# Optimization experiments

Hardware: AMD Instinct MI355X
Metric: run time of the kernel (lower is better)

The kernel has to match this reference:

```python
import jax, jax.numpy as jnp
import numpy as np

# (multiplicity, irrep dim 2l+1, is_scalar) for '128x0e + 64x1o + 32x2e'
IRREPS = [(128, 1, True), (64, 3, False), (32, 5, False)]
EPS = 1e-05
NUM_GRAPHS = 64


def setup_inputs() -> dict:
    key = jax.random.key(0)
    k1, k2 = jax.random.split(key)
    N, dim = 200000, 480
    x = jax.random.normal(k1, (N, dim), dtype=jnp.float32)
    batch_id = jnp.sort(jax.random.randint(k2, (N,), 0, NUM_GRAPHS)).astype(jnp.int64)
    weight = jnp.ones((224,), dtype=jnp.float32)   # per-irrep-channel scale
    bias = jnp.zeros((128,), dtype=jnp.float32)    # scalar channels only
    return {"input": x, "batch_id_tensor": batch_id, "weight": weight, "bias": bias}


def _segment_mean(vals, seg, num_segments):
    # vals: (N, mul) -> per-graph mean (G, mul)
    sums = jax.ops.segment_sum(vals, seg, num_segments=num_segments)
    counts = jax.ops.segment_sum(jnp.ones((vals.shape[0],), vals.dtype), seg,
                                 num_segments=num_segments)
    return sums / jnp.maximum(counts, 1.0)[:, None]


def reference(input, batch_id_tensor, weight, bias):
    N = input.shape[0]
    seg = batch_id_tensor.astype(jnp.int32)
    ix = iw = ib = 0
    outs = []
    for mul, d, is_scalar in IRREPS:
        f = input[:, ix:ix + mul * d].reshape(N, mul, d)
        ix += mul * d
        if is_scalar:
            # instance norm: per-graph mean of scalar channels, gathered back
            m = _segment_mean(f[:, :, 0], seg, NUM_GRAPHS)[seg]  # (N, mul)
            f = f - m[:, :, None]
        # 'component' normalization: mean of squares over irrep dim
        fn = jnp.mean(f * f, axis=2)                             # (N, mul)
        # reduce='mean' over (trivial) spatial axis, then per-graph mean
        fn = _segment_mean(fn, seg, NUM_GRAPHS)[seg]             # (N, mul)
        fn = (fn + EPS) ** -0.5 * weight[iw:iw + mul]
        iw += mul
        f = f * fn[:, :, None]
        if is_scalar:
            f = f + bias[ib:ib + mul][:, None]
            ib += mul
        outs.append(f.reshape(N, mul * d))
    return jnp.concatenate(outs, axis=1)
```

## Files before the change

kernel.cpp:

```cpp
#include <hip/hip_runtime.h>

#define NGRAPHS 64
#define DIM 480
#define NCH 224
#define EPS 1e-5f
#define TILE 128

typedef float f32x4 __attribute__((ext_vector_type(4)));

#define OFF_SSQ   0
#define OFF_SUM   14336
#define OFF_START 22528
#define OFF_TPRE  22593
#define ZN_FLOATS 22528

__device__ __forceinline__ int col2ch(int col) {
    if (col < 128) return col;
    if (col < 320) return 128 + (col - 128) / 3;
    return 192 + (col - 320) / 5;
}

__global__ __launch_bounds__(256) void init_kernel(const int* __restrict__ bid,
                                                   float* __restrict__ ws, int N) {
    int b = blockIdx.x;
    if (b < 88) {
        int i = b * 256 + threadIdx.x;
        if (i < ZN_FLOATS) ws[i] = 0.0f;
        return;
    }
    int* start = (int*)(ws + OFF_START);
    int* tpre  = (int*)(ws + OFF_TPRE);
    int g = threadIdx.x;
    if (g <= NGRAPHS) {
        int lo = 0, hi = N;
        while (lo < hi) { int mid = (lo + hi) >> 1; if (bid[mid] < g) lo = mid + 1; else hi = mid; }
        start[g] = lo;
    }
    __syncthreads();
    if (threadIdx.x == 0) {
        int acc = 0;
        for (int gg = 0; gg < NGRAPHS; ++gg) {
            tpre[gg] = acc;
            acc += (start[gg + 1] - start[gg] + TILE - 1) / TILE;
        }
        tpre[NGRAPHS] = acc;
    }
}

__device__ __forceinline__ void block_tile(const int* __restrict__ tpre, int b,
                                           int& g, int& tile) {
    int lo = 0, hi = NGRAPHS;
    while (hi - lo > 1) {
        int mid = (lo + hi) >> 1;
        if (tpre[mid] <= b) lo = mid; else hi = mid;
    }
    g = lo;
    tile = b - tpre[lo];
}

__device__ __forceinline__ void flush_quad(float* __restrict__ SQ, int col0,
                                           float v0, float v1, float v2, float v3) {
    float v[4] = {v0, v1, v2, v3};
    int ch0 = col2ch(col0), ch1 = col2ch(col0 + 1),
        ch2 = col2ch(col0 + 2), ch3 = col2ch(col0 + 3);
    float acc = v[0]; int cur = ch0;
    if (ch1 == cur) acc += v[1]; else { atomicAdd(&SQ[cur], acc); cur = ch1; acc = v[1]; }
    if (ch2 == cur) acc += v[2]; else { atomicAdd(&SQ[cur], acc); cur = ch2; acc = v[2]; }
    if (ch3 == cur) acc += v[3]; else { atomicAdd(&SQ[cur], acc); cur = ch3; acc = v[3]; }
    atomicAdd(&SQ[cur], acc);
}

__global__ __launch_bounds__(256) void stats_kernel(const float* __restrict__ x,
                                                    float* __restrict__ ws) {
    __shared__ float red[256][13];
    const int* start = (const int*)(ws + OFF_START);
    const int* tpre  = (const int*)(ws + OFF_TPRE);
    if ((int)blockIdx.x >= tpre[NGRAPHS]) return;
    int g, tile;
    block_tile(tpre, blockIdx.x, g, tile);
    int r0 = start[g] + tile * TILE;
    int r1 = min(r0 + TILE, start[g + 1]);

    const int t  = threadIdx.x;
    const int tx = t & 63;
    const int ty = t >> 6;

    float ssq[8]  = {0, 0, 0, 0, 0, 0, 0, 0};
    float ssum[4] = {0, 0, 0, 0};
    for (int r = r0 + ty; r < r1; r += 4) {
        const float4* rowp = (const float4*)(x + (size_t)r * DIM);
        float4 v0 = rowp[tx];
        ssq[0] += v0.x * v0.x; ssq[1] += v0.y * v0.y;
        ssq[2] += v0.z * v0.z; ssq[3] += v0.w * v0.w;
        if (tx < 32) {
            ssum[0] += v0.x; ssum[1] += v0.y; ssum[2] += v0.z; ssum[3] += v0.w;
        }
        if (tx < 56) {
            float4 v1 = rowp[64 + tx];
            ssq[4] += v1.x * v1.x; ssq[5] += v1.y * v1.y;
            ssq[6] += v1.z * v1.z; ssq[7] += v1.w * v1.w;
        }
    }

#pragma unroll
    for (int j = 0; j < 8; ++j) red[t][j] = ssq[j];
#pragma unroll
    for (int j = 0; j < 4; ++j) red[t][8 + j] = ssum[j];
    __syncthreads();
    if (ty == 0) {
        float s[8], sm[4];
#pragma unroll
        for (int j = 0; j < 8; ++j)
            s[j] = red[tx][j] + red[tx + 64][j] + red[tx + 128][j] + red[tx + 192][j];
#pragma unroll
        for (int j = 0; j < 4; ++j)
            sm[j] = red[tx][8 + j] + red[tx + 64][8 + j] + red[tx + 128][8 + j] + red[tx + 192][8 + j];
        float* SQ = ws + OFF_SSQ + (size_t)g * NCH;
        float* SM = ws + OFF_SUM + (size_t)g * 128;
        flush_quad(SQ, 4 * tx, s[0], s[1], s[2], s[3]);
        if (tx < 32) {
#pragma unroll
            for (int j = 0; j < 4; ++j) atomicAdd(&SM[4 * tx + j], sm[j]);
        }
        if (tx < 56) flush_quad(SQ, 256 + 4 * tx, s[4], s[5], s[6], s[7]);
    }
}

__global__ __launch_bounds__(256) void norm_kernel(const float* __restrict__ x,
                                                   const float* __restrict__ w,
                                                   const float* __restrict__ bias,
                                                   const float* __restrict__ ws,
                                                   float* __restrict__ out) {
    const int* start = (const int*)(ws + OFF_START);
    const int* tpre  = (const int*)(ws + OFF_TPRE);
    int total = tpre[NGRAPHS];
    int b = total - 1 - (int)blockIdx.x;
    if (b < 0) return;
    int t = threadIdx.x;
    if (t >= 240) return;
    int g, tile;
    block_tile(tpre, b, g, tile);
    int r0 = start[g] + tile * TILE;
    int r1 = min(r0 + TILE, start[g + 1]);

    int row_off = t / 120;
    int c4 = t - row_off * 120;

    float cnt = (float)max(start[g + 1] - start[g], 1);
    const float* SQ = ws + OFF_SSQ + (size_t)g * NCH;
    const float* SM = ws + OFF_SUM + (size_t)g * 128;

    float A[4], B[4];
#pragma unroll
    for (int j = 0; j < 4; ++j) {
        int col = 4 * c4 + j;
        int ch = col2ch(col);
        float ssq = SQ[ch];
        if (col < 128) {
            float m   = SM[col] / cnt;
            float var = ssq / cnt - m * m;
            float Av  = rsqrtf(var + EPS) * w[ch];
            A[j] = Av;
            B[j] = bias[col] - m * Av;
        } else {
            float d = (col < 320) ? 3.0f : 5.0f;
            A[j] = rsqrtf(ssq / (d * cnt) + EPS) * w[ch];
            B[j] = 0.0f;
        }
    }

    const float4* xp = (const float4*)(x + (size_t)(r0 + row_off) * DIM) + c4;
    f32x4*        op = (f32x4*)(out + (size_t)(r0 + row_off) * DIM + 4 * c4);
    const int stride4 = 2 * (DIM / 4);
    for (int r = r0 + row_off; r < r1; r += 2) {
        float4 xv = *xp;
        f32x4 o;
        o.x = xv.x * A[0] + B[0];
        o.y = xv.y * A[1] + B[1];
        o.z = xv.z * A[2] + B[2];
        o.w = xv.w * A[3] + B[3];
        *op = o;
        xp += stride4;
        op += stride4;
    }
}

extern "C" void kernel_launch(void* const* d_in, const int* in_sizes, int n_in,
                              void* d_out, int out_size, void* d_ws, size_t ws_size,
                              hipStream_t stream) {
    const float* x   = (const float*)d_in[0];
    const int*   bid = (const int*)d_in[1];
    const float* w   = (const float*)d_in[2];
    const float* b   = (const float*)d_in[3];
    float* ws  = (float*)d_ws;
    float* out = (float*)d_out;
    int N = in_sizes[1];
    int ntiles_ub = (N + TILE - 1) / TILE + NGRAPHS;

    init_kernel<<<89, 256, 0, stream>>>(bid, ws, N);
    stats_kernel<<<ntiles_ub, 256, 0, stream>>>(x, ws);
    norm_kernel<<<ntiles_ub, 256, 0, stream>>>(x, w, b, ws, out);
}
```

Before: 273.2 us.

## Fuse stats and normalization into one persistent kernel with per-graph spin barrier

Replaces the init, stats and norm launches with a single kernel that launches 16 blocks per graph. Each block computes partial sums for its slice of rows and writes them to a per-block slot, then waits on a per-graph counter until all 16 slots are in. After that the block reduces the partials and normalizes the same rows it just read, which it expects to still find in cache. Output stores become nontemporal. The design needs all 1024 blocks to be co-resident for the spin barrier to be safe, has a bounded spin fallback, and loses load balance across graphs of uneven size.

```diff
diff --git a/kernel.cpp b/kernel.cpp
--- a/kernel.cpp
+++ b/kernel.cpp
@@ -4,21 +4,157 @@
 #define DIM 480
 #define NCH 224
 #define EPS 1e-5f
+#define SLOTS 16
+#define PSTR 640
+#define SPIN_BOUND (1u << 24)
 #define TILE 128
 
 typedef float f32x4 __attribute__((ext_vector_type(4)));
+
+__device__ __forceinline__ int col2ch(int col) {
+    if (col < 128) return col;
+    if (col < 320) return 128 + (col - 128) / 3;
+    return 192 + (col - 320) / 5;
+}
+
+__global__ __launch_bounds__(256, 4) void fused_kernel(
+        const float* __restrict__ x, const int* __restrict__ bid,
+        const float* __restrict__ w, const float* __restrict__ bias,
+        unsigned int* __restrict__ done, float* __restrict__ part,
+        float* __restrict__ out, int N) {
+    __shared__ int s_se[2];
+    __shared__ float red[256][13];
+    __shared__ float lds_col[608];
+
+    const int t  = threadIdx.x;
+    const int g  = blockIdx.x >> 4;
+    const int js = blockIdx.x & (SLOTS - 1);
+
+    if (t < 2) {
+        int target = g + t, lo = 0, hi = N;
+        while (lo < hi) { int mid = (lo + hi) >> 1; if (bid[mid] < target) lo = mid + 1; else hi = mid; }
+        s_se[t] = lo;
+    }
+    __syncthreads();
+    const int rs = s_se[0], re = s_se[1];
+    const int cnt_i = re - rs;
+    const int chunk = (cnt_i + SLOTS - 1) / SLOTS;
+    const int r0s = rs + js * chunk;
+    const int r1s = min(r0s + chunk, re);
+
+    const int tx = t & 63;
+    const int ty = t >> 6;
+
+    float ssq[8]  = {0, 0, 0, 0, 0, 0, 0, 0};
+    float ssum[4] = {0, 0, 0, 0};
+    for (int r = r0s + ty; r < r1s; r += 4) {
+        const float4* rowp = (const float4*)(x + (size_t)r * DIM);
+        float4 v0 = rowp[tx];
+        ssq[0] += v0.x * v0.x; ssq[1] += v0.y * v0.y;
+        ssq[2] += v0.z * v0.z; ssq[3] += v0.w * v0.w;
+        if (tx < 32) { ssum[0] += v0.x; ssum[1] += v0.y; ssum[2] += v0.z; ssum[3] += v0.w; }
+        if (tx < 56) {
+            float4 v1 = rowp[64 + tx];
+            ssq[4] += v1.x * v1.x; ssq[5] += v1.y * v1.y;
+            ssq[6] += v1.z * v1.z; ssq[7] += v1.w * v1.w;
+        }
+    }
+#pragma unroll
+    for (int j = 0; j < 8; ++j) red[t][j] = ssq[j];
+#pragma unroll
+    for (int j = 0; j < 4; ++j) red[t][8 + j] = ssum[j];
+    __syncthreads();
+    if (ty == 0) {
+        float* P = part + (size_t)blockIdx.x * PSTR;
+#pragma unroll
+        for (int j = 0; j < 8; ++j) ssq[j] = red[tx][j] + red[tx + 64][j] + red[tx + 128][j] + red[tx + 192][j];
+#pragma unroll
+        for (int j = 0; j < 4; ++j) ssum[j] = red[tx][8 + j] + red[tx + 64][8 + j] + red[tx + 128][8 + j] + red[tx + 192][8 + j];
+#pragma unroll
+        for (int j = 0; j < 4; ++j)
+            __hip_atomic_store(&P[4 * tx + j], ssq[j], __ATOMIC_RELAXED, __HIP_MEMORY_SCOPE_AGENT);
+        if (tx < 56) {
+#pragma unroll
+            for (int j = 0; j < 4; ++j)
+                __hip_atomic_store(&P[256 + 4 * tx + j], ssq[4 + j], __ATOMIC_RELAXED, __HIP_MEMORY_SCOPE_AGENT);
+        }
+        if (tx < 32) {
+#pragma unroll
+            for (int j = 0; j < 4; ++j)
+                __hip_atomic_store(&P[480 + 4 * tx + j], ssum[j], __ATOMIC_RELAXED, __HIP_MEMORY_SCOPE_AGENT);
+        }
+    }
+    __syncthreads();
+
+    if (t == 0) {
+        __hip_atomic_fetch_add(&done[g], 1u, __ATOMIC_RELEASE, __HIP_MEMORY_SCOPE_AGENT);
+        unsigned it = 0;
+        while (__hip_atomic_load(&done[g], __ATOMIC_ACQUIRE, __HIP_MEMORY_SCOPE_AGENT) < SLOTS) {
+            if (++it > SPIN_BOUND) break;
+            __builtin_amdgcn_s_sleep(32);
+        }
+    }
+    __syncthreads();
+
+    const float* Pg = part + (size_t)g * SLOTS * PSTR;
+    for (int col = t; col < 608; col += 256) {
+        float a = 0.0f;
+        for (int s = 0; s < SLOTS; ++s)
+            a += __hip_atomic_load(&Pg[(size_t)s * PSTR + col], __ATOMIC_RELAXED, __HIP_MEMORY_SCOPE_AGENT);
+        lds_col[col] = a;
+    }
+    __syncthreads();
+
+    if (t < 240) {
+        const int row_off = t / 120;
+        const int c4 = t - row_off * 120;
+        float cnt = (float)max(cnt_i, 1);
+        float A[4], B[4];
+#pragma unroll
+        for (int j = 0; j < 4; ++j) {
+            int col = 4 * c4 + j;
+            if (col < 128) {
+                float m   = lds_col[480 + col] / cnt;
+                float var = lds_col[col] / cnt - m * m;
+                float Av  = rsqrtf(var + EPS) * w[col];
+                A[j] = Av;
+                B[j] = bias[col] - m * Av;
+            } else if (col < 320) {
+                int k = (col - 128) / 3, c0 = 128 + 3 * k;
+                float sq = lds_col[c0] + lds_col[c0 + 1] + lds_col[c0 + 2];
+                A[j] = rsqrtf(sq / (3.0f * cnt) + EPS) * w[128 + k];
+                B[j] = 0.0f;
+            } else {
+                int k = (col - 320) / 5, c0 = 320 + 5 * k;
+                float sq = lds_col[c0] + lds_col[c0 + 1] + lds_col[c0 + 2]
+                         + lds_col[c0 + 3] + lds_col[c0 + 4];
+                A[j] = rsqrtf(sq / (5.0f * cnt) + EPS) * w[192 + k];
+                B[j] = 0.0f;
+            }
+        }
+        const float4* xp = (const float4*)(x + (size_t)(r0s + row_off) * DIM) + c4;
+        float*        op = out + (size_t)(r0s + row_off) * DIM + 4 * c4;
+        const int stride4 = 2 * (DIM / 4);
+        const int strideF = 2 * DIM;
+        for (int r = r0s + row_off; r < r1s; r += 2) {
+            float4 xv = *xp;
+            f32x4 o;
+            o.x = xv.x * A[0] + B[0];
+            o.y = xv.y * A[1] + B[1];
+            o.z = xv.z * A[2] + B[2];
+            o.w = xv.w * A[3] + B[3];
+            __builtin_nontemporal_store(o, (f32x4*)op);
+            xp += stride4;
+            op += strideF;
+        }
+    }
+}
 
 #define OFF_SSQ   0
 #define OFF_SUM   14336
 #define OFF_START 22528
 #define OFF_TPRE  22593
 #define ZN_FLOATS 22528
-
-__device__ __forceinline__ int col2ch(int col) {
-    if (col < 128) return col;
-    if (col < 320) return 128 + (col - 128) / 3;
-    return 192 + (col - 320) / 5;
-}
 
 __global__ __launch_bounds__(256) void init_kernel(const int* __restrict__ bid,
                                                    float* __restrict__ ws, int N) {
@@ -50,10 +186,7 @@
 __device__ __forceinline__ void block_tile(const int* __restrict__ tpre, int b,
                                            int& g, int& tile) {
     int lo = 0, hi = NGRAPHS;
-    while (hi - lo > 1) {
-        int mid = (lo + hi) >> 1;
-        if (tpre[mid] <= b) lo = mid; else hi = mid;
-    }
+    while (hi - lo > 1) { int mid = (lo + hi) >> 1; if (tpre[mid] <= b) lo = mid; else hi = mid; }
     g = lo;
     tile = b - tpre[lo];
 }
@@ -80,28 +213,18 @@
     block_tile(tpre, blockIdx.x, g, tile);
     int r0 = start[g] + tile * TILE;
     int r1 = min(r0 + TILE, start[g + 1]);
-
-    const int t  = threadIdx.x;
-    const int tx = t & 63;
-    const int ty = t >> 6;
-
-    float ssq[8]  = {0, 0, 0, 0, 0, 0, 0, 0};
-    float ssum[4] = {0, 0, 0, 0};
+    const int t = threadIdx.x, tx = t & 63, ty = t >> 6;
+    float ssq[8] = {0,0,0,0,0,0,0,0}, ssum[4] = {0,0,0,0};
     for (int r = r0 + ty; r < r1; r += 4) {
         const float4* rowp = (const float4*)(x + (size_t)r * DIM);
         float4 v0 = rowp[tx];
-        ssq[0] += v0.x * v0.x; ssq[1] += v0.y * v0.y;
-        ssq[2] += v0.z * v0.z; ssq[3] += v0.w * v0.w;
-        if (tx < 32) {
-            ssum[0] += v0.x; ssum[1] += v0.y; ssum[2] += v0.z; ssum[3] += v0.w;
-        }
+        ssq[0] += v0.x*v0.x; ssq[1] += v0.y*v0.y; ssq[2] += v0.z*v0.z; ssq[3] += v0.w*v0.w;
+        if (tx < 32) { ssum[0] += v0.x; ssum[1] += v0.y; ssum[2] += v0.z; ssum[3] += v0.w; }
         if (tx < 56) {
             float4 v1 = rowp[64 + tx];
-            ssq[4] += v1.x * v1.x; ssq[5] += v1.y * v1.y;
-            ssq[6] += v1.z * v1.z; ssq[7] += v1.w * v1.w;
-        }
-    }
-
+            ssq[4] += v1.x*v1.x; ssq[5] += v1.y*v1.y; ssq[6] += v1.z*v1.z; ssq[7] += v1.w*v1.w;
+        }
+    }
 #pragma unroll
     for (int j = 0; j < 8; ++j) red[t][j] = ssq[j];
 #pragma unroll
@@ -142,14 +265,10 @@
     block_tile(tpre, b, g, tile);
     int r0 = start[g] + tile * TILE;
     int r1 = min(r0 + TILE, start[g + 1]);
-
-    int row_off = t / 120;
-    int c4 = t - row_off * 120;
-
+    int row_off = t / 120, c4 = t - row_off * 120;
     float cnt = (float)max(start[g + 1] - start[g], 1);
     const float* SQ = ws + OFF_SSQ + (size_t)g * NCH;
     const float* SM = ws + OFF_SUM + (size_t)g * 128;
-
     float A[4], B[4];
 #pragma unroll
     for (int j = 0; j < 4; ++j) {
@@ -157,21 +276,20 @@
         int ch = col2ch(col);
         float ssq = SQ[ch];
         if (col < 128) {
-            float m   = SM[col] / cnt;
+            float m = SM[col] / cnt;
             float var = ssq / cnt - m * m;
-            float Av  = rsqrtf(var + EPS) * w[ch];
-            A[j] = Av;
-            B[j] = bias[col] - m * Av;
+            float Av = rsqrtf(var + EPS) * w[ch];
+            A[j] = Av; B[j] = bias[col] - m * Av;
         } else {
             float d = (col < 320) ? 3.0f : 5.0f;
             A[j] = rsqrtf(ssq / (d * cnt) + EPS) * w[ch];
             B[j] = 0.0f;
         }
     }
-
     const float4* xp = (const float4*)(x + (size_t)(r0 + row_off) * DIM) + c4;
-    f32x4*        op = (f32x4*)(out + (size_t)(r0 + row_off) * DIM + 4 * c4);
+    float*        op = out + (size_t)(r0 + row_off) * DIM + 4 * c4;
     const int stride4 = 2 * (DIM / 4);
+    const int strideF = 2 * DIM;
     for (int r = r0 + row_off; r < r1; r += 2) {
         float4 xv = *xp;
         f32x4 o;
@@ -179,9 +297,9 @@
         o.y = xv.y * A[1] + B[1];
         o.z = xv.z * A[2] + B[2];
         o.w = xv.w * A[3] + B[3];
-        *op = o;
+        __builtin_nontemporal_store(o, (f32x4*)op);
         xp += stride4;
-        op += stride4;
+        op += strideF;
     }
 }
 
@@ -195,9 +313,17 @@
     float* ws  = (float*)d_ws;
     float* out = (float*)d_out;
     int N = in_sizes[1];
-    int ntiles_ub = (N + TILE - 1) / TILE + NGRAPHS;
-
-    init_kernel<<<89, 256, 0, stream>>>(bid, ws, N);
-    stats_kernel<<<ntiles_ub, 256, 0, stream>>>(x, ws);
-    norm_kernel<<<ntiles_ub, 256, 0, stream>>>(x, w, b, ws, out);
-}
+
+    size_t need = 64 * sizeof(unsigned) + (size_t)NGRAPHS * SLOTS * PSTR * sizeof(float);
+    if (ws_size >= need) {
+        hipMemsetAsync(ws, 0, 64 * sizeof(unsigned), stream);
+        unsigned* done = (unsigned*)ws;
+        float* part = ws + 64;
+        fused_kernel<<<NGRAPHS * SLOTS, 256, 0, stream>>>(x, bid, w, b, done, part, out, N);
+    } else {
+        int ntiles_ub = (N + TILE - 1) / TILE + NGRAPHS;
+        init_kernel<<<89, 256, 0, stream>>>(bid, ws, N);
+        stats_kernel<<<ntiles_ub, 256, 0, stream>>>(x, ws);
+        norm_kernel<<<ntiles_ub, 256, 0, stream>>>(x, w, b, ws, out);
+    }
+}
```

Result: slower. 323.3 us (+18.4%).

## Split graphs into halves and overlap normalize of first half with stats of second

Applied to the files above, without the earlier changes.

Reorganizes the two-pass pipeline into three launches. The first computes stats for graphs 0-31. The second normalizes graphs 0-31 while computing stats for graphs 32-63. The third normalizes graphs 32-63. This aims to cut the tail/idle time between the stats and norm phases and to keep x for the first half warm in cache. Output stores also switch to nontemporal stores to avoid polluting the cache, at the cost of an extra kernel launch and mixed block types in the middle kernel.

```diff
diff --git a/kernel.cpp b/kernel.cpp
--- a/kernel.cpp
+++ b/kernel.cpp
@@ -70,38 +70,28 @@
     atomicAdd(&SQ[cur], acc);
 }
 
-__global__ __launch_bounds__(256) void stats_kernel(const float* __restrict__ x,
-                                                    float* __restrict__ ws) {
-    __shared__ float red[256][13];
-    const int* start = (const int*)(ws + OFF_START);
-    const int* tpre  = (const int*)(ws + OFF_TPRE);
-    if ((int)blockIdx.x >= tpre[NGRAPHS]) return;
+
+__device__ __forceinline__ void stats_tile_body(const float* __restrict__ x,
+                                                float* __restrict__ ws,
+                                                const int* __restrict__ start,
+                                                const int* __restrict__ tpre,
+                                                int b, float (*red)[13]) {
     int g, tile;
-    block_tile(tpre, blockIdx.x, g, tile);
+    block_tile(tpre, b, g, tile);
     int r0 = start[g] + tile * TILE;
     int r1 = min(r0 + TILE, start[g + 1]);
-
-    const int t  = threadIdx.x;
-    const int tx = t & 63;
-    const int ty = t >> 6;
-
-    float ssq[8]  = {0, 0, 0, 0, 0, 0, 0, 0};
-    float ssum[4] = {0, 0, 0, 0};
+    const int t = threadIdx.x, tx = t & 63, ty = t >> 6;
+    float ssq[8] = {0,0,0,0,0,0,0,0}, ssum[4] = {0,0,0,0};
     for (int r = r0 + ty; r < r1; r += 4) {
         const float4* rowp = (const float4*)(x + (size_t)r * DIM);
         float4 v0 = rowp[tx];
-        ssq[0] += v0.x * v0.x; ssq[1] += v0.y * v0.y;
-        ssq[2] += v0.z * v0.z; ssq[3] += v0.w * v0.w;
-        if (tx < 32) {
-            ssum[0] += v0.x; ssum[1] += v0.y; ssum[2] += v0.z; ssum[3] += v0.w;
-        }
+        ssq[0] += v0.x*v0.x; ssq[1] += v0.y*v0.y; ssq[2] += v0.z*v0.z; ssq[3] += v0.w*v0.w;
+        if (tx < 32) { ssum[0] += v0.x; ssum[1] += v0.y; ssum[2] += v0.z; ssum[3] += v0.w; }
         if (tx < 56) {
             float4 v1 = rowp[64 + tx];
-            ssq[4] += v1.x * v1.x; ssq[5] += v1.y * v1.y;
-            ssq[6] += v1.z * v1.z; ssq[7] += v1.w * v1.w;
-        }
-    }
-
+            ssq[4] += v1.x*v1.x; ssq[5] += v1.y*v1.y; ssq[6] += v1.z*v1.z; ssq[7] += v1.w*v1.w;
+        }
+    }
 #pragma unroll
     for (int j = 0; j < 8; ++j) red[t][j] = ssq[j];
 #pragma unroll
@@ -126,30 +116,23 @@
     }
 }
 
-__global__ __launch_bounds__(256) void norm_kernel(const float* __restrict__ x,
-                                                   const float* __restrict__ w,
-                                                   const float* __restrict__ bias,
-                                                   const float* __restrict__ ws,
-                                                   float* __restrict__ out) {
-    const int* start = (const int*)(ws + OFF_START);
-    const int* tpre  = (const int*)(ws + OFF_TPRE);
-    int total = tpre[NGRAPHS];
-    int b = total - 1 - (int)blockIdx.x;
-    if (b < 0) return;
+__device__ __forceinline__ void norm_tile_body(const float* __restrict__ x,
+                                               const float* __restrict__ w,
+                                               const float* __restrict__ bias,
+                                               const float* __restrict__ ws,
+                                               float* __restrict__ out,
+                                               const int* __restrict__ start,
+                                               const int* __restrict__ tpre, int b) {
     int t = threadIdx.x;
     if (t >= 240) return;
     int g, tile;
     block_tile(tpre, b, g, tile);
     int r0 = start[g] + tile * TILE;
     int r1 = min(r0 + TILE, start[g + 1]);
-
-    int row_off = t / 120;
-    int c4 = t - row_off * 120;
-
+    int row_off = t / 120, c4 = t - row_off * 120;
     float cnt = (float)max(start[g + 1] - start[g], 1);
     const float* SQ = ws + OFF_SSQ + (size_t)g * NCH;
     const float* SM = ws + OFF_SUM + (size_t)g * 128;
-
     float A[4], B[4];
 #pragma unroll
     for (int j = 0; j < 4; ++j) {
@@ -157,21 +140,20 @@
         int ch = col2ch(col);
         float ssq = SQ[ch];
         if (col < 128) {
-            float m   = SM[col] / cnt;
+            float m = SM[col] / cnt;
             float var = ssq / cnt - m * m;
-            float Av  = rsqrtf(var + EPS) * w[ch];
-            A[j] = Av;
-            B[j] = bias[col] - m * Av;
+            float Av = rsqrtf(var + EPS) * w[ch];
+            A[j] = Av; B[j] = bias[col] - m * Av;
         } else {
             float d = (col < 320) ? 3.0f : 5.0f;
             A[j] = rsqrtf(ssq / (d * cnt) + EPS) * w[ch];
             B[j] = 0.0f;
         }
     }
-
     const float4* xp = (const float4*)(x + (size_t)(r0 + row_off) * DIM) + c4;
-    f32x4*        op = (f32x4*)(out + (size_t)(r0 + row_off) * DIM + 4 * c4);
+    float*        op = out + (size_t)(r0 + row_off) * DIM + 4 * c4;
     const int stride4 = 2 * (DIM / 4);
+    const int strideF = 2 * DIM;
     for (int r = r0 + row_off; r < r1; r += 2) {
         float4 xv = *xp;
         f32x4 o;
@@ -179,10 +161,50 @@
         o.y = xv.y * A[1] + B[1];
         o.z = xv.z * A[2] + B[2];
         o.w = xv.w * A[3] + B[3];
-        *op = o;
+        __builtin_nontemporal_store(o, (f32x4*)op);
         xp += stride4;
-        op += stride4;
-    }
+        op += strideF;
+    }
+}
+
+__global__ __launch_bounds__(256) void stats_lo_kernel(const float* __restrict__ x,
+                                                       float* __restrict__ ws) {
+    __shared__ float red[256][13];
+    const int* start = (const int*)(ws + OFF_START);
+    const int* tpre  = (const int*)(ws + OFF_TPRE);
+    int b = blockIdx.x;
+    if (b >= tpre[32]) return;
+    stats_tile_body(x, ws, start, tpre, b, red);
+}
+
+__global__ __launch_bounds__(256) void mixed_kernel(const float* __restrict__ x,
+                                                    const float* __restrict__ w,
+                                                    const float* __restrict__ bias,
+                                                    float* __restrict__ ws,
+                                                    float* __restrict__ out) {
+    __shared__ float red[256][13];
+    const int* start = (const int*)(ws + OFF_START);
+    const int* tpre  = (const int*)(ws + OFF_TPRE);
+    int T0 = tpre[32], T1 = tpre[NGRAPHS];
+    int bb = blockIdx.x;
+    if (bb < T0) {
+        norm_tile_body(x, w, bias, ws, out, start, tpre, T0 - 1 - bb);
+    } else if (bb < T1) {
+        stats_tile_body(x, ws, start, tpre, bb, red);
+    }
+}
+
+__global__ __launch_bounds__(256) void norm_hi_kernel(const float* __restrict__ x,
+                                                      const float* __restrict__ w,
+                                                      const float* __restrict__ bias,
+                                                      const float* __restrict__ ws,
+                                                      float* __restrict__ out) {
+    const int* start = (const int*)(ws + OFF_START);
+    const int* tpre  = (const int*)(ws + OFF_TPRE);
+    int T0 = tpre[32], T1 = tpre[NGRAPHS];
+    int b = T1 - 1 - (int)blockIdx.x;
+    if (b < T0) return;
+    norm_tile_body(x, w, bias, ws, out, start, tpre, b);
 }
 
 extern "C" void kernel_launch(void* const* d_in, const int* in_sizes, int n_in,
@@ -198,6 +220,7 @@
     int ntiles_ub = (N + TILE - 1) / TILE + NGRAPHS;
 
     init_kernel<<<89, 256, 0, stream>>>(bid, ws, N);
-    stats_kernel<<<ntiles_ub, 256, 0, stream>>>(x, ws);
-    norm_kernel<<<ntiles_ub, 256, 0, stream>>>(x, w, b, ws, out);
-}
+    stats_lo_kernel<<<ntiles_ub, 256, 0, stream>>>(x, ws);
+    mixed_kernel<<<ntiles_ub, 256, 0, stream>>>(x, w, b, ws, out);
+    norm_hi_kernel<<<ntiles_ub, 256, 0, stream>>>(x, w, b, ws, out);
+}
```

New measurement: 258.8 us. 5.2% less time.
